# Kernel tuning notes

Hardware: AMD Instinct MI355X
Metric: run time of the kernel (lower is better)

The kernel has to match this reference:

```python
import jax, jax.numpy as jnp
import numpy as np

N, IN_DIM, OUT_DIM = 8192, 512, 256


def setup_inputs() -> dict:
    key = jax.random.key(0)
    k1, k2, k3, k4 = jax.random.split(key, 4)
    x = jax.random.normal(k1, (N, IN_DIM), dtype=jnp.float32)
    adj = jax.random.randint(k2, (N, N), 0, 2, dtype=jnp.int32)
    # nn.Linear(in_dim, out_dim, bias=False).weight -> [out_dim, in_dim]
    W_proj = jax.random.normal(k3, (OUT_DIM, IN_DIM), dtype=jnp.float32) * (1.0 / np.sqrt(IN_DIM))
    # nn.Linear(2*out_dim, 1, bias=False).weight flattened -> [2*out_dim]
    a = jax.random.normal(k4, (2 * OUT_DIM,), dtype=jnp.float32) * (1.0 / np.sqrt(2 * OUT_DIM))
    return {"x": x, "adj": adj, "W_proj": W_proj, "a": a}


def reference(x, adj, W_proj, a):
    # h = proj(x): [N, D]
    h = x @ W_proj.T
    D = h.shape[-1]
    # attn(cat([h_i, h_j])) == h_i @ a[:D] + h_j @ a[D:]  (exact decomposition,
    # avoids materializing the [N, N, 2D] concat tensor)
    s_i = h @ a[:D]   # [N]
    s_j = h @ a[D:]   # [N]
    scores = s_i[:, None] + s_j[None, :]          # [N, N]
    scores = jnp.where(adj > 0, scores, -jnp.inf)  # masked_fill
    alpha = jax.nn.softmax(scores, axis=1)         # softmax over neighbors j
    # dropout is identity in eval mode
    out = alpha @ h                                # [N, D]
    return jax.nn.elu(out), alpha
```

## Files before the change

kernel.cpp:

```cpp
#include <hip/hip_runtime.h>
#include <hip/hip_bf16.h>

#define NR 8192
#define DIN 512
#define DD 256

typedef __attribute__((ext_vector_type(8))) short short8;
typedef __attribute__((ext_vector_type(4))) float f32x4;
typedef __attribute__((ext_vector_type(2))) unsigned long long u64x2;

static __device__ __forceinline__ unsigned short f2bf(float x) {
    __hip_bfloat16 b = __float2bfloat16(x);
    return __builtin_bit_cast(unsigned short, b);
}
static __device__ __forceinline__ float bf2f(unsigned short u) {
    unsigned v = ((unsigned)u) << 16;
    return __builtin_bit_cast(float, v);
}

static __device__ __forceinline__ short8 frag_from_byte(
        const unsigned long long* __restrict__ lut, unsigned b) {
    u64x2 t;
    t.x = lut[b & 15u];
    t.y = lut[(b >> 4) & 15u];
    return __builtin_bit_cast(short8, t);
}

__global__ __launch_bounds__(256) void k_gemm_h(
        const float* __restrict__ x, const float* __restrict__ W,
        float* __restrict__ h) {
    __shared__ unsigned short Ah[64][72], Al[64][72];
    __shared__ unsigned short Bh[128][72], Bl[128][72];
    const int t = threadIdx.x;
    const int i0 = blockIdx.x * 64;
    const int n0 = blockIdx.y * 128;
    const int lane = t & 63, q = lane >> 4, lm = lane & 15;
    const int w = t >> 6, wm = w >> 1, wn = w & 1;
    const int ar = t >> 2, ac0 = (t & 3) << 4;
    const int bn = t >> 1, bh0 = (t & 1) << 5;
    f32x4 acc[2][4];
#pragma unroll
    for (int mt = 0; mt < 2; ++mt)
#pragma unroll
        for (int nt = 0; nt < 4; ++nt) acc[mt][nt] = (f32x4){0.f, 0.f, 0.f, 0.f};

    for (int kb = 0; kb < DIN; kb += 64) {
        __syncthreads();
        {
            const float4* xp = (const float4*)(x + (size_t)(i0 + ar) * DIN + kb + ac0);
#pragma unroll
            for (int u = 0; u < 4; ++u) {
                float4 v = xp[u];
                unsigned short h0 = f2bf(v.x), h1 = f2bf(v.y), h2 = f2bf(v.z), h3 = f2bf(v.w);
                unsigned short l0 = f2bf(v.x - bf2f(h0)), l1 = f2bf(v.y - bf2f(h1));
                unsigned short l2 = f2bf(v.z - bf2f(h2)), l3 = f2bf(v.w - bf2f(h3));
                *(uint2*)&Ah[ar][ac0 + u * 4] =
                    make_uint2((unsigned)h0 | ((unsigned)h1 << 16), (unsigned)h2 | ((unsigned)h3 << 16));
                *(uint2*)&Al[ar][ac0 + u * 4] =
                    make_uint2((unsigned)l0 | ((unsigned)l1 << 16), (unsigned)l2 | ((unsigned)l3 << 16));
            }
            const float4* wp = (const float4*)(W + (size_t)(n0 + bn) * DIN + kb + bh0);
#pragma unroll
            for (int u = 0; u < 8; ++u) {
                float4 v = wp[u];
                unsigned short h0 = f2bf(v.x), h1 = f2bf(v.y), h2 = f2bf(v.z), h3 = f2bf(v.w);
                unsigned short l0 = f2bf(v.x - bf2f(h0)), l1 = f2bf(v.y - bf2f(h1));
                unsigned short l2 = f2bf(v.z - bf2f(h2)), l3 = f2bf(v.w - bf2f(h3));
                *(uint2*)&Bh[bn][bh0 + u * 4] =
                    make_uint2((unsigned)h0 | ((unsigned)h1 << 16), (unsigned)h2 | ((unsigned)h3 << 16));
                *(uint2*)&Bl[bn][bh0 + u * 4] =
                    make_uint2((unsigned)l0 | ((unsigned)l1 << 16), (unsigned)l2 | ((unsigned)l3 << 16));
            }
        }
        __syncthreads();
#pragma unroll
        for (int ks = 0; ks < 64; ks += 32) {
            short8 fa_h[2], fa_l[2], fb_h[4], fb_l[4];
#pragma unroll
            for (int mt = 0; mt < 2; ++mt) {
                int r = wm * 32 + mt * 16 + lm;
                fa_h[mt] = *(const short8*)&Ah[r][ks + q * 8];
                fa_l[mt] = *(const short8*)&Al[r][ks + q * 8];
            }
#pragma unroll
            for (int nt = 0; nt < 4; ++nt) {
                int c = wn * 64 + nt * 16 + lm;
                fb_h[nt] = *(const short8*)&Bh[c][ks + q * 8];
                fb_l[nt] = *(const short8*)&Bl[c][ks + q * 8];
            }
#pragma unroll
            for (int mt = 0; mt < 2; ++mt)
#pragma unroll
                for (int nt = 0; nt < 4; ++nt) {
                    acc[mt][nt] = __builtin_amdgcn_mfma_f32_16x16x32_bf16(fa_h[mt], fb_h[nt], acc[mt][nt], 0, 0, 0);
                    acc[mt][nt] = __builtin_amdgcn_mfma_f32_16x16x32_bf16(fa_h[mt], fb_l[nt], acc[mt][nt], 0, 0, 0);
                    acc[mt][nt] = __builtin_amdgcn_mfma_f32_16x16x32_bf16(fa_l[mt], fb_h[nt], acc[mt][nt], 0, 0, 0);
                }
        }
    }
#pragma unroll
    for (int mt = 0; mt < 2; ++mt)
#pragma unroll
        for (int nt = 0; nt < 4; ++nt)
#pragma unroll
            for (int rr = 0; rr < 4; ++rr) {
                int row = i0 + wm * 32 + mt * 16 + q * 4 + rr;
                int col = n0 + wn * 64 + nt * 16 + lm;
                h[(size_t)row * DD + col] = acc[mt][nt][rr];
            }
}

__global__ __launch_bounds__(256) void k_s(
        const float* __restrict__ h, const float* __restrict__ a,
        float* __restrict__ s, float* __restrict__ pmax) {
    __shared__ float wmax[4];
    const int t = threadIdx.x, w = t >> 6, lane = t & 63;
    const int row = blockIdx.x * 4 + w;
    float4 hv = *(const float4*)(h + (size_t)row * DD + lane * 4);
    float4 av = *(const float4*)(a + DD + lane * 4);
    float d = hv.x * av.x + hv.y * av.y + hv.z * av.z + hv.w * av.w;
#pragma unroll
    for (int off = 32; off; off >>= 1) d += __shfl_down(d, off);
    if (lane == 0) { s[row] = d; wmax[w] = d; }
    __syncthreads();
    if (t == 0)
        pmax[blockIdx.x] = fmaxf(fmaxf(wmax[0], wmax[1]), fmaxf(wmax[2], wmax[3]));
}

__global__ __launch_bounds__(1024) void k_e(
        const float* __restrict__ s, const float* __restrict__ pmax,
        float* __restrict__ e) {
    __shared__ float red[1024];
    const int t = threadIdx.x;
    red[t] = fmaxf(pmax[t], pmax[t + 1024]);
    __syncthreads();
    for (int off = 512; off; off >>= 1) {
        if (t < off) red[t] = fmaxf(red[t], red[t + off]);
        __syncthreads();
    }
    float M = red[0];
    for (int j = t; j < NR; j += 1024) e[j] = expf(s[j] - M);
}

__global__ __launch_bounds__(256) void k_gt(
        const float* __restrict__ h, const float* __restrict__ e,
        unsigned short* __restrict__ gt) {
    __shared__ float tile[64][68];
    const int t = threadIdx.x;
    const int j0 = blockIdx.x * 64, d0 = blockIdx.y * 64;
    const int r = t >> 4, c4 = (t & 15) * 4;
#pragma unroll
    for (int rr = 0; rr < 4; ++rr) {
        int row = r + rr * 16;
        *(float4*)&tile[row][c4] = *(const float4*)(h + (size_t)(j0 + row) * DD + d0 + c4);
    }
    __syncthreads();
    float4 ev = *(const float4*)(e + j0 + c4);
#pragma unroll
    for (int rr = 0; rr < 4; ++rr) {
        int dd = r + rr * 16;
        unsigned short o0 = f2bf(ev.x * tile[c4 + 0][dd]);
        unsigned short o1 = f2bf(ev.y * tile[c4 + 1][dd]);
        unsigned short o2 = f2bf(ev.z * tile[c4 + 2][dd]);
        unsigned short o3 = f2bf(ev.w * tile[c4 + 3][dd]);
        *(uint2*)(gt + (size_t)(d0 + dd) * NR + j0 + c4) =
            make_uint2((unsigned)o0 | ((unsigned)o1 << 16), (unsigned)o2 | ((unsigned)o3 << 16));
    }
}

__global__ __launch_bounds__(1024) void k_fused(
        const int* __restrict__ adj, const unsigned short* __restrict__ gt,
        const float* __restrict__ e, float* __restrict__ out0,
        float* __restrict__ alpha) {
    __shared__ __attribute__((aligned(16))) unsigned char bm[32768];
    __shared__ unsigned long long lut[16];
    __shared__ float dnm_s[32];
    __shared__ int chunk_cnt[16];
    __shared__ int dnm_ready;

    const int t = threadIdx.x;
    const int row0 = blockIdx.x * 32;
    const int lane = t & 63, w = t >> 6;

    if (t < 16) {
        unsigned long long v = 0;
        if (t & 1) v |= 0x3F80ull;
        if (t & 2) v |= 0x3F80ull << 16;
        if (t & 4) v |= 0x3F80ull << 32;
        if (t & 8) v |= 0x3F80ull << 48;
        lut[t] = v;
        chunk_cnt[t] = 0;
    }
    if (t == 16) dnm_ready = 0;
    __syncthreads();

    if (w < 8) {
        const int r0 = w * 4;
        const int* __restrict__ ap0 = adj + (size_t)(row0 + r0) * NR;
        float ds0 = 0.f, ds1 = 0.f, ds2 = 0.f, ds3 = 0.f;

        for (int ch = 0; ch < 16; ++ch) {
#pragma unroll
            for (int g = 0; g < 2; ++g) {
                const int itc0 = ch * 8 + g * 4;
                int v[4][4];
                float ec[4];
#pragma unroll
                for (int u = 0; u < 4; ++u) ec[u] = e[(itc0 + u) * 64 + lane];
#pragma unroll
                for (int rr = 0; rr < 4; ++rr)
#pragma unroll
                    for (int u = 0; u < 4; ++u)
                        v[rr][u] = __builtin_nontemporal_load(
                            ap0 + (size_t)rr * NR + (itc0 + u) * 64 + lane);
#pragma unroll
                for (int u = 0; u < 4; ++u) {
                    unsigned long long b0 = __ballot(v[0][u] != 0);
                    unsigned long long b1 = __ballot(v[1][u] != 0);
                    unsigned long long b2 = __ballot(v[2][u] != 0);
                    unsigned long long b3 = __ballot(v[3][u] != 0);
                    ds0 += v[0][u] ? ec[u] : 0.f;
                    ds1 += v[1][u] ? ec[u] : 0.f;
                    ds2 += v[2][u] ? ec[u] : 0.f;
                    ds3 += v[3][u] ? ec[u] : 0.f;
                    if (lane < 4) {
                        unsigned long long bv = lane == 0 ? b0 :
                                                lane == 1 ? b1 :
                                                lane == 2 ? b2 : b3;
                        const int r = r0 + lane;
                        *(unsigned long long*)&bm[
                            (unsigned)(r * 1024 + (itc0 + u) * 8) ^
                            ((unsigned)(r & 7) << 4)] = bv;
                    }
                }
            }
            if (lane == 0)
                __hip_atomic_fetch_add(&chunk_cnt[ch], 1, __ATOMIC_RELEASE,
                                       __HIP_MEMORY_SCOPE_WORKGROUP);
        }
#pragma unroll
        for (int off = 32; off; off >>= 1) {
            ds0 += __shfl_xor(ds0, off);
            ds1 += __shfl_xor(ds1, off);
            ds2 += __shfl_xor(ds2, off);
            ds3 += __shfl_xor(ds3, off);
        }
        const float inv0 = 1.f / ds0, inv1 = 1.f / ds1;
        const float inv2 = 1.f / ds2, inv3 = 1.f / ds3;
        if (lane == 0) {
            dnm_s[r0 + 0] = inv0;
            dnm_s[r0 + 1] = inv1;
            dnm_s[r0 + 2] = inv2;
            dnm_s[r0 + 3] = inv3;
        }
        if (lane == 0)
            __hip_atomic_fetch_add(&dnm_ready, 1, __ATOMIC_RELEASE,
                                   __HIP_MEMORY_SCOPE_WORKGROUP);

        float* __restrict__ al0 = alpha + (size_t)(row0 + r0) * NR;
        const int bof = lane >> 3, bsh = lane & 7;
#pragma unroll 2
        for (int itc = 0; itc < 128; ++itc) {
            const int col = itc * 64 + lane;
            const float ec = e[col];
#pragma unroll
            for (int rr = 0; rr < 4; ++rr) {
                const int r = r0 + rr;
                unsigned byte = bm[(unsigned)(r * 1024 + itc * 8 + bof) ^
                                   ((unsigned)(r & 7) << 4)];
                const float inv = rr == 0 ? inv0 : rr == 1 ? inv1 :
                                  rr == 2 ? inv2 : inv3;
                float val = ((byte >> bsh) & 1u) ? ec * inv : 0.f;
                __builtin_nontemporal_store(val, al0 + (size_t)rr * NR + col);
            }
        }
    } else {
        const int cw = w - 8;
        const int q = lane >> 4, lm = lane & 15;
        const int qs = q * 8;
        const unsigned bswz = (unsigned)((lm & 7) << 4);
        const int b0base = lm * 1024;
        const int b1base = (16 + lm) * 1024;

        const unsigned short* __restrict__ gb0 =
            gt + (size_t)(cw * 32 + lm) * NR + q * 8;
        const unsigned short* __restrict__ gb1 =
            gt + (size_t)(cw * 32 + 16 + lm) * NR + q * 8;

        f32x4 acc[2][2];
#pragma unroll
        for (int mt = 0; mt < 2; ++mt)
#pragma unroll
            for (int nt = 0; nt < 2; ++nt) acc[mt][nt] = (f32x4){0.f, 0.f, 0.f, 0.f};

#define LOADK(B, KO) do {                                                      \
        B[0] = *(const short8*)(gb0 + (KO));                                   \
        B[1] = *(const short8*)(gb0 + (KO) + 32);                              \
        B[2] = *(const short8*)(gb0 + (KO) + 64);                              \
        B[3] = *(const short8*)(gb0 + (KO) + 96);                              \
        B[4] = *(const short8*)(gb1 + (KO));                                   \
        B[5] = *(const short8*)(gb1 + (KO) + 32);                              \
        B[6] = *(const short8*)(gb1 + (KO) + 64);                              \
        B[7] = *(const short8*)(gb1 + (KO) + 96);                              \
    } while (0)

#define SSTEP(B, S, W0, W1) do {                                               \
        short8 fa0 = frag_from_byte(lut, ((W0) >> qs) & 0xFFu);                \
        short8 fa1 = frag_from_byte(lut, ((W1) >> qs) & 0xFFu);                \
        acc[0][0] = __builtin_amdgcn_mfma_f32_16x16x32_bf16(fa0, B[S], acc[0][0], 0, 0, 0);     \
        acc[1][0] = __builtin_amdgcn_mfma_f32_16x16x32_bf16(fa1, B[S], acc[1][0], 0, 0, 0);     \
        acc[0][1] = __builtin_amdgcn_mfma_f32_16x16x32_bf16(fa0, B[4 + S], acc[0][1], 0, 0, 0); \
        acc[1][1] = __builtin_amdgcn_mfma_f32_16x16x32_bf16(fa1, B[4 + S], acc[1][1], 0, 0, 0); \
    } while (0)

#define CSTEP(B, M0, M1) do {                                                  \
        SSTEP(B, 0, (M0).x, (M1).x);                                           \
        SSTEP(B, 1, (M0).y, (M1).y);                                           \
        SSTEP(B, 2, (M0).z, (M1).z);                                           \
        SSTEP(B, 3, (M0).w, (M1).w);                                           \
    } while (0)

        short8 bA[8], bB[8];
        LOADK(bA, 0);
        for (int ch = 0; ch < 16; ++ch) {
            while (__hip_atomic_load(&chunk_cnt[ch], __ATOMIC_ACQUIRE,
                                     __HIP_MEMORY_SCOPE_WORKGROUP) < 8)
                __builtin_amdgcn_s_sleep(1);
            const int kt0 = ch * 4;
#pragma unroll
            for (int k2 = 0; k2 < 4; k2 += 2) {
                const int kt = kt0 + k2;
                uint4 m0a = *(const uint4*)&bm[(unsigned)(b0base + kt * 16) ^ bswz];
                uint4 m1a = *(const uint4*)&bm[(unsigned)(b1base + kt * 16) ^ bswz];
                LOADK(bB, (kt + 1) * 128);
                CSTEP(bA, m0a, m1a);
                uint4 m0b = *(const uint4*)&bm[(unsigned)(b0base + (kt + 1) * 16) ^ bswz];
                uint4 m1b = *(const uint4*)&bm[(unsigned)(b1base + (kt + 1) * 16) ^ bswz];
                if (kt + 2 < 64) LOADK(bA, (kt + 2) * 128);
                CSTEP(bB, m0b, m1b);
            }
        }
#undef LOADK
#undef SSTEP
#undef CSTEP

        while (__hip_atomic_load(&dnm_ready, __ATOMIC_ACQUIRE,
                                 __HIP_MEMORY_SCOPE_WORKGROUP) < 8)
            __builtin_amdgcn_s_sleep(1);
#pragma unroll
        for (int mt = 0; mt < 2; ++mt)
#pragma unroll
            for (int nt = 0; nt < 2; ++nt)
#pragma unroll
                for (int rr = 0; rr < 4; ++rr) {
                    const int rrow = mt * 16 + q * 4 + rr;
                    float z = acc[mt][nt][rr] * dnm_s[rrow];
                    float oo = z > 0.f ? z : expm1f(z);
                    __builtin_nontemporal_store(oo,
                        &out0[(size_t)(row0 + rrow) * DD + cw * 32 + nt * 16 + lm]);
                }
    }
}

extern "C" void kernel_launch(void* const* d_in, const int* in_sizes, int n_in,
                              void* d_out, int out_size, void* d_ws, size_t ws_size,
                              hipStream_t stream) {
    const float* x = (const float*)d_in[0];
    const int* adj = (const int*)d_in[1];
    const float* W = (const float*)d_in[2];
    const float* a = (const float*)d_in[3];
    float* out0 = (float*)d_out;
    float* alpha = (float*)d_out + (size_t)NR * DD;

    char* ws = (char*)d_ws;
    float* h            = (float*)(ws + 0);
    float* s            = (float*)(ws + 8388608);
    float* pmax         = (float*)(ws + 8421376);
    float* e            = (float*)(ws + 8429568);
    unsigned short* gt  = (unsigned short*)(ws + 8462336);

    k_gemm_h<<<dim3(128, 2), 256, 0, stream>>>(x, W, h);
    k_s<<<2048, 256, 0, stream>>>(h, a, s, pmax);
    k_e<<<1, 1024, 0, stream>>>(s, pmax, e);
    k_gt<<<dim3(128, 4), 256, 0, stream>>>(h, e, gt);
    k_fused<<<256, 1024, 0, stream>>>(adj, gt, e, out0, alpha);
}
```

Measured before the change: 539.7 us.

## Double-buffer adjacency loads and split alpha writes across producer and MFMA waves

The adjacency scan now loads 8-column chunks into two alternating register buffers, issuing the next chunk's loads before processing the current one so memory latency is hidden. The alpha-row writeback is split: producer waves write two of their four rows, and the compute (MFMA) waves write the other two after finishing the output tile. This balances the large alpha store traffic across more waves, at the cost of higher register pressure from the doubled buffers. It also puts extra tail work on the compute waves.

```diff
diff --git a/kernel.cpp b/kernel.cpp
--- a/kernel.cpp
+++ b/kernel.cpp
@@ -199,45 +199,57 @@
         const int* __restrict__ ap0 = adj + (size_t)(row0 + r0) * NR;
         float ds0 = 0.f, ds1 = 0.f, ds2 = 0.f, ds3 = 0.f;
 
-        for (int ch = 0; ch < 16; ++ch) {
-#pragma unroll
-            for (int g = 0; g < 2; ++g) {
-                const int itc0 = ch * 8 + g * 4;
-                int v[4][4];
-                float ec[4];
-#pragma unroll
-                for (int u = 0; u < 4; ++u) ec[u] = e[(itc0 + u) * 64 + lane];
-#pragma unroll
-                for (int rr = 0; rr < 4; ++rr)
-#pragma unroll
-                    for (int u = 0; u < 4; ++u)
-                        v[rr][u] = __builtin_nontemporal_load(
-                            ap0 + (size_t)rr * NR + (itc0 + u) * 64 + lane);
-#pragma unroll
-                for (int u = 0; u < 4; ++u) {
-                    unsigned long long b0 = __ballot(v[0][u] != 0);
-                    unsigned long long b1 = __ballot(v[1][u] != 0);
-                    unsigned long long b2 = __ballot(v[2][u] != 0);
-                    unsigned long long b3 = __ballot(v[3][u] != 0);
-                    ds0 += v[0][u] ? ec[u] : 0.f;
-                    ds1 += v[1][u] ? ec[u] : 0.f;
-                    ds2 += v[2][u] ? ec[u] : 0.f;
-                    ds3 += v[3][u] ? ec[u] : 0.f;
-                    if (lane < 4) {
-                        unsigned long long bv = lane == 0 ? b0 :
-                                                lane == 1 ? b1 :
-                                                lane == 2 ? b2 : b3;
-                        const int r = r0 + lane;
-                        *(unsigned long long*)&bm[
-                            (unsigned)(r * 1024 + (itc0 + u) * 8) ^
-                            ((unsigned)(r & 7) << 4)] = bv;
-                    }
-                }
-            }
-            if (lane == 0)
-                __hip_atomic_fetch_add(&chunk_cnt[ch], 1, __ATOMIC_RELEASE,
-                                       __HIP_MEMORY_SCOPE_WORKGROUP);
-        }
+#define PLOAD(VV, EE, CH) do {                                                 \
+        const int _i0 = (CH) * 8;                                              \
+        _Pragma("unroll")                                                      \
+        for (int u = 0; u < 8; ++u) EE[u] = e[(_i0 + u) * 64 + lane];          \
+        _Pragma("unroll")                                                      \
+        for (int rr = 0; rr < 4; ++rr)                                         \
+            _Pragma("unroll")                                                  \
+            for (int u = 0; u < 8; ++u)                                        \
+                VV[rr][u] = __builtin_nontemporal_load(                        \
+                    ap0 + (size_t)rr * NR + (_i0 + u) * 64 + lane);            \
+    } while (0)
+
+#define PPROC(VV, EE, CH) do {                                                 \
+        const int _i0 = (CH) * 8;                                              \
+        _Pragma("unroll")                                                      \
+        for (int u = 0; u < 8; ++u) {                                          \
+            unsigned long long b0 = __ballot(VV[0][u] != 0);                   \
+            unsigned long long b1 = __ballot(VV[1][u] != 0);                   \
+            unsigned long long b2 = __ballot(VV[2][u] != 0);                   \
+            unsigned long long b3 = __ballot(VV[3][u] != 0);                   \
+            ds0 += VV[0][u] ? EE[u] : 0.f;                                     \
+            ds1 += VV[1][u] ? EE[u] : 0.f;                                     \
+            ds2 += VV[2][u] ? EE[u] : 0.f;                                     \
+            ds3 += VV[3][u] ? EE[u] : 0.f;                                     \
+            if (lane < 4) {                                                    \
+                unsigned long long bv = lane == 0 ? b0 : lane == 1 ? b1 :      \
+                                        lane == 2 ? b2 : b3;                   \
+                const int r = r0 + lane;                                       \
+                *(unsigned long long*)&bm[(unsigned)(r * 1024 + (_i0 + u) * 8) \
+                                          ^ ((unsigned)(r & 7) << 4)] = bv;    \
+            }                                                                  \
+        }                                                                      \
+        if (lane == 0)                                                         \
+            __hip_atomic_fetch_add(&chunk_cnt[CH], 1, __ATOMIC_RELEASE,        \
+                                   __HIP_MEMORY_SCOPE_WORKGROUP);              \
+    } while (0)
+
+        {
+            int vA[4][8], vB[4][8];
+            float eA[8], eB[8];
+            PLOAD(vA, eA, 0);
+            for (int ch = 0; ch < 16; ch += 2) {
+                PLOAD(vB, eB, ch + 1);
+                PPROC(vA, eA, ch);
+                if (ch + 2 < 16) PLOAD(vA, eA, ch + 2);
+                PPROC(vB, eB, ch + 1);
+            }
+        }
+#undef PLOAD
+#undef PPROC
+
 #pragma unroll
         for (int off = 32; off; off >>= 1) {
             ds0 += __shfl_xor(ds0, off);
@@ -252,26 +264,26 @@
             dnm_s[r0 + 1] = inv1;
             dnm_s[r0 + 2] = inv2;
             dnm_s[r0 + 3] = inv3;
-        }
-        if (lane == 0)
             __hip_atomic_fetch_add(&dnm_ready, 1, __ATOMIC_RELEASE,
                                    __HIP_MEMORY_SCOPE_WORKGROUP);
-
-        float* __restrict__ al0 = alpha + (size_t)(row0 + r0) * NR;
-        const int bof = lane >> 3, bsh = lane & 7;
-#pragma unroll 2
-        for (int itc = 0; itc < 128; ++itc) {
-            const int col = itc * 64 + lane;
-            const float ec = e[col];
-#pragma unroll
-            for (int rr = 0; rr < 4; ++rr) {
-                const int r = r0 + rr;
-                unsigned byte = bm[(unsigned)(r * 1024 + itc * 8 + bof) ^
-                                   ((unsigned)(r & 7) << 4)];
-                const float inv = rr == 0 ? inv0 : rr == 1 ? inv1 :
-                                  rr == 2 ? inv2 : inv3;
-                float val = ((byte >> bsh) & 1u) ? ec * inv : 0.f;
-                __builtin_nontemporal_store(val, al0 + (size_t)rr * NR + col);
+        }
+
+        {
+            float* __restrict__ al0 = alpha + (size_t)(row0 + r0) * NR;
+            float* __restrict__ al1 = al0 + NR;
+            const int bof = lane >> 3, bsh = lane & 7;
+            const unsigned sz0 = (unsigned)((r0 & 7) << 4);
+            const unsigned sz1 = (unsigned)(((r0 + 1) & 7) << 4);
+#pragma unroll 4
+            for (int itc = 0; itc < 128; ++itc) {
+                const int col = itc * 64 + lane;
+                const float ecv = e[col];
+                unsigned by0 = bm[(unsigned)(r0 * 1024 + itc * 8 + bof) ^ sz0];
+                unsigned by1 = bm[(unsigned)((r0 + 1) * 1024 + itc * 8 + bof) ^ sz1];
+                __builtin_nontemporal_store(
+                    ((by0 >> bsh) & 1u) ? ecv * inv0 : 0.f, al0 + col);
+                __builtin_nontemporal_store(
+                    ((by1 >> bsh) & 1u) ? ecv * inv1 : 0.f, al1 + col);
             }
         }
     } else {
@@ -359,6 +371,27 @@
                     __builtin_nontemporal_store(oo,
                         &out0[(size_t)(row0 + rrow) * DD + cw * 32 + nt * 16 + lm]);
                 }
+
+        {
+            const int ra0 = cw * 4 + 2;
+            const float invA = dnm_s[ra0], invB = dnm_s[ra0 + 1];
+            float* __restrict__ aw0 = alpha + (size_t)(row0 + ra0) * NR;
+            float* __restrict__ aw1 = aw0 + NR;
+            const int bof = lane >> 3, bsh = lane & 7;
+            const unsigned szA = (unsigned)((ra0 & 7) << 4);
+            const unsigned szB = (unsigned)(((ra0 + 1) & 7) << 4);
+#pragma unroll 4
+            for (int itc = 0; itc < 128; ++itc) {
+                const int col = itc * 64 + lane;
+                const float ecv = e[col];
+                unsigned byA = bm[(unsigned)(ra0 * 1024 + itc * 8 + bof) ^ szA];
+                unsigned byB = bm[(unsigned)((ra0 + 1) * 1024 + itc * 8 + bof) ^ szB];
+                __builtin_nontemporal_store(
+                    ((byA >> bsh) & 1u) ? ecv * invA : 0.f, aw0 + col);
+                __builtin_nontemporal_store(
+                    ((byB >> bsh) & 1u) ? ecv * invB : 0.f, aw1 + col);
+            }
+        }
     }
 }
 
```

Result: slower. 561.6 us (+4.0%).
